# Kernel tuning notes

Measured on AMD Instinct MI355X. Metric: run time of the kernel, lower is better.

## Reference

```python
import jax, jax.numpy as jnp
import numpy as np

N, D = 4096, 512
TAU, ALPHA, EPS = 0.2, 0.5, 1e-15
L2_EPS = 1e-12  # F.normalize eps


def setup_inputs() -> dict:
    key = jax.random.key(0)
    ks = jax.random.split(key, 12)
    # xavier_normal_ with gain=1.414 for [D, D] linears
    std = 1.414 * (2.0 / (D + D)) ** 0.5
    xn = lambda k: jax.random.normal(k, (D, D), jnp.float32) * std
    return {
        "z1": jax.random.normal(ks[0], (N, D), jnp.float32),
        "z2": jax.random.normal(ks[1], (N, D), jnp.float32),
        # local projector: Linear -> PReLU -> Linear
        "lw1": xn(ks[2]), "lb1": jnp.zeros((D,), jnp.float32),
        "la": jnp.full((1,), 0.25, jnp.float32),  # PReLU weight (torch default 0.25)
        "lw2": xn(ks[3]), "lb2": jnp.zeros((D,), jnp.float32),
        # global projector
        "gw1": xn(ks[4]), "gb1": jnp.zeros((D,), jnp.float32),
        "ga": jnp.full((1,), 0.25, jnp.float32),
        "gw2": xn(ks[5]), "gb2": jnp.zeros((D,), jnp.float32),
        # discriminator bilinear weight
        "W": xn(ks[6]),
        # binary positive-pair mask [N, N]
        "mask": jax.random.randint(ks[7], (N, N), 0, 2, jnp.int32),
    }


def _prelu(x, a):
    return jnp.where(x >= 0, x, a * x)


def _proj(z, w1, b1, a, w2, b2):
    # nn.Sequential(Linear, PReLU, Linear); torch Linear: z @ W.T + b
    return _prelu(z @ w1.T + b1, a[0]) @ w2.T + b2


def _l2norm(z):
    n = jnp.linalg.norm(z, axis=-1, keepdims=True)
    return z / jnp.maximum(n, L2_EPS)


def _infonce(h1, h2, m, tau):
    a = _l2norm(h1)
    b = _l2norm(h2)
    sim_intra = jnp.exp(a @ a.T / tau)  # [N, N]
    sim_inter = jnp.exp(a @ b.T / tau)  # [N, N]
    num = (sim_inter * m).sum(1)
    den = sim_intra.sum(1) + sim_inter.sum(1) - (sim_intra * m).sum(1)
    return (-jnp.log(num / den)).mean()


def reference(z1, z2, lw1, lb1, la, lw2, lb2, gw1, gb1, ga, gw2, gb2, W, mask):
    m = mask.astype(jnp.float32)
    # local (node-level) InfoNCE through the local projector
    h1 = _proj(z1, lw1, lb1, la, lw2, lb2)
    h2 = _proj(z2, lw1, lb1, la, lw2, lb2)
    local = 0.5 * (_infonce(h1, h2, m, TAU) + _infonce(h2, h1, m.T, TAU))

    # global (DGI-style) loss
    def gloss(pos_z, neg_z):
        s = pos_z.mean(0)                               # readout [D]
        h = _proj(s, gw1, gb1, ga, gw2, gb2)            # global projector [D]
        summ = W @ h                                    # [D]
        d_pos = jax.nn.sigmoid(pos_z @ summ)            # [N]
        d_neg = jax.nn.sigmoid(neg_z @ summ)            # [N]
        pos_loss = -jnp.log(d_pos + EPS).mean()
        neg_loss = -jnp.log(1.0 - d_neg + EPS).mean()
        return 0.5 * (pos_loss + neg_loss)

    glob = 0.5 * (gloss(z1, z2) + gloss(z2, z1))
    return ALPHA * local + (1.0 - ALPHA) * glob
```

## Files before the change

### kernel.cpp

```cpp
#include <hip/hip_runtime.h>
#include <math.h>

#define NN 4096
#define DD 512
#define INV_TAU 5.0f
#define EPSV 1e-15f

typedef unsigned short u16;
typedef __attribute__((ext_vector_type(8))) short short8;
typedef __attribute__((ext_vector_type(4))) float f32x4;

__device__ __forceinline__ void gld16(const void* g, void* l) {
  __builtin_amdgcn_global_load_lds(
      (const __attribute__((address_space(1))) unsigned int*)g,
      (__attribute__((address_space(3))) unsigned int*)l, 16, 0, 0);
}

__device__ __forceinline__ float bf2f(u16 u) {
  return __uint_as_float(((unsigned)u) << 16);
}
__device__ __forceinline__ u16 f2bf(float x) {
  unsigned u = __float_as_uint(x);
  u += 0x7fff + ((u >> 16) & 1);
  return (u16)(u >> 16);
}

__device__ __forceinline__ float wave_sum(float v) {
#pragma unroll
  for (int o = 32; o > 0; o >>= 1) v += __shfl_down(v, o, 64);
  return v;
}

__global__ __launch_bounds__(256) void tobf16_2(const float* __restrict__ a,
                                                const float* __restrict__ b,
                                                u16* __restrict__ d,
                                                int n4each) {
  const int i = blockIdx.x * 256 + threadIdx.x;
  const float* s =
      (i < n4each) ? a + (size_t)i * 4 : b + (size_t)(i - n4each) * 4;
  float4 v = *(const float4*)s;
  unsigned long long pk = (unsigned long long)f2bf(v.x) |
                          ((unsigned long long)f2bf(v.y) << 16) |
                          ((unsigned long long)f2bf(v.z) << 32) |
                          ((unsigned long long)f2bf(v.w) << 48);
  *(unsigned long long*)&d[(size_t)i * 4] = pk;
}

template <int ACT>
__global__ __launch_bounds__(256) void gemm_mfma(
    const u16* __restrict__ A, const u16* __restrict__ Bw,
    const float* __restrict__ bias, const float* __restrict__ alpha_p,
    u16* __restrict__ out) {
  __shared__ __align__(16) u16 sA[2][128 * 32], sB[2][128 * 32];
  const int tid = threadIdx.x, w = tid >> 6, lane = tid & 63;
  const int rq = lane >> 2, cq = (lane & 3) * 8;
  const int quad = lane >> 4, m16 = lane & 15;
  const int wi = w >> 1, wj = w & 1;
  const int i0 = blockIdx.y * 128, j0 = blockIdx.x * 128;
  const u16* Ab = A + (size_t)blockIdx.z * ((size_t)NN * DD);
  u16* ob = out + (size_t)blockIdx.z * ((size_t)NN * DD);
  const int p = w >> 1, rh = (w & 1) * 64;
  const u16* gs = p ? Bw : Ab;
  const int grow0 = (p ? j0 : i0) + rh + rq;
  u16* lb0 = p ? &sB[0][rh * 32] : &sA[0][rh * 32];
  u16* lb1 = p ? &sB[1][rh * 32] : &sA[1][rh * 32];
#pragma unroll
  for (int rr = 0; rr < 64; rr += 16)
    gld16(&gs[(size_t)(grow0 + rr) * DD + cq], lb0 + rr * 32);
  f32x4 acc[4][4] = {};
  for (int kc = 0; kc < 16; ++kc) {
    __syncthreads();
    if (kc < 15) {
      const int kn = (kc + 1) * 32;
      u16* d = (kc & 1) ? lb0 : lb1;
#pragma unroll
      for (int rr = 0; rr < 64; rr += 16)
        gld16(&gs[(size_t)(grow0 + rr) * DD + kn + cq], d + rr * 32);
    }
    const u16* As = sA[kc & 1];
    const u16* Bs = sB[kc & 1];
    short8 ar[4], br[4];
#pragma unroll
    for (int s = 0; s < 4; ++s) {
      ar[s] = *(const short8*)&As[(wi * 64 + s * 16 + m16) * 32 + quad * 8];
      br[s] = *(const short8*)&Bs[(wj * 64 + s * 16 + m16) * 32 + quad * 8];
    }
#pragma unroll
    for (int si = 0; si < 4; ++si)
#pragma unroll
      for (int sj = 0; sj < 4; ++sj)
        acc[si][sj] = __builtin_amdgcn_mfma_f32_16x16x32_bf16(
            ar[si], br[sj], acc[si][sj], 0, 0, 0);
  }
  const float al = ACT ? alpha_p[0] : 0.f;
#pragma unroll
  for (int si = 0; si < 4; ++si)
#pragma unroll
    for (int sj = 0; sj < 4; ++sj) {
      const int col = j0 + wj * 64 + sj * 16 + m16;
      const float bv = bias[col];
#pragma unroll
      for (int r = 0; r < 4; ++r) {
        const int row = i0 + wi * 64 + si * 16 + quad * 4 + r;
        float x = acc[si][sj][r] + bv;
        if (ACT) x = (x >= 0.f) ? x : al * x;
        ob[(size_t)row * DD + col] = f2bf(x);
      }
    }
}

__global__ __launch_bounds__(256) void rownorm_bf16(const u16* __restrict__ h,
                                                    u16* __restrict__ o) {
  const int row = blockIdx.x;
  const int t = threadIdx.x;
  const size_t base = (size_t)row * DD;
  float v0 = bf2f(h[base + t]);
  float v1 = bf2f(h[base + 256 + t]);
  float s = v0 * v0 + v1 * v1;
  s = wave_sum(s);
  __shared__ float wsum[4];
  const int lane = t & 63, wid = t >> 6;
  if (lane == 0) wsum[wid] = s;
  __syncthreads();
  if (t == 0) {
    float tot = wsum[0] + wsum[1] + wsum[2] + wsum[3];
    wsum[0] = 1.f / fmaxf(sqrtf(tot), 1e-12f);
  }
  __syncthreads();
  const float inv = wsum[0];
  o[base + t] = f2bf(v0 * inv);
  o[base + 256 + t] = f2bf(v1 * inv);
}

__global__ __launch_bounds__(512) void sim_mfma(
    const u16* __restrict__ na, const u16* __restrict__ nb,
    const int* __restrict__ mask, float* __restrict__ zb) {
  __shared__ __align__(16) u16 sP[2][4][128 * 32];
  const int tid = threadIdx.x;
  const int w = tid >> 6, lane = tid & 63;
  const int rq = lane >> 2, cq = (lane & 3) * 8;
  const int quad = lane >> 4, m16 = lane & 15;
  const int ig = w & 3, jh = w >> 2;
  const int i0 = blockIdx.y * 128, j0 = blockIdx.x * 128;
  const int p = w >> 1, rh = (w & 1) * 64;
  const u16* gs = (p & 1) ? nb : na;
  const int grow0 = ((p < 2) ? i0 : j0) + rh + rq;
  u16* lb0 = &sP[0][p][rh * 32];
  u16* lb1 = &sP[1][p][rh * 32];
#pragma unroll
  for (int rr = 0; rr < 64; rr += 16)
    gld16(&gs[(size_t)(grow0 + rr) * DD + cq], lb0 + rr * 32);
  f32x4 a11[2][4] = {}, a12[2][4] = {}, a22[2][4] = {};
  for (int kc = 0; kc < 16; ++kc) {
    __syncthreads();
    if (kc < 15) {
      const int kn = (kc + 1) * 32;
      u16* d = (kc & 1) ? lb0 : lb1;
#pragma unroll
      for (int rr = 0; rr < 64; rr += 16)
        gld16(&gs[(size_t)(grow0 + rr) * DD + kn + cq], d + rr * 32);
    }
    const u16* Ai = sP[kc & 1][0];
    const u16* Bi = sP[kc & 1][1];
    const u16* Aj = sP[kc & 1][2];
    const u16* Bj = sP[kc & 1][3];
    short8 ai0 = *(const short8*)&Ai[(ig * 32 + m16) * 32 + quad * 8];
    short8 ai1 = *(const short8*)&Ai[(ig * 32 + 16 + m16) * 32 + quad * 8];
    short8 bi0 = *(const short8*)&Bi[(ig * 32 + m16) * 32 + quad * 8];
    short8 bi1 = *(const short8*)&Bi[(ig * 32 + 16 + m16) * 32 + quad * 8];
#pragma unroll
    for (int c = 0; c < 4; ++c) {
      short8 aj = *(const short8*)&Aj[(jh * 64 + c * 16 + m16) * 32 + quad * 8];
      short8 bj = *(const short8*)&Bj[(jh * 64 + c * 16 + m16) * 32 + quad * 8];
      a11[0][c] = __builtin_amdgcn_mfma_f32_16x16x32_bf16(ai0, aj, a11[0][c], 0, 0, 0);
      a11[1][c] = __builtin_amdgcn_mfma_f32_16x16x32_bf16(ai1, aj, a11[1][c], 0, 0, 0);
      a12[0][c] = __builtin_amdgcn_mfma_f32_16x16x32_bf16(ai0, bj, a12[0][c], 0, 0, 0);
      a12[1][c] = __builtin_amdgcn_mfma_f32_16x16x32_bf16(ai1, bj, a12[1][c], 0, 0, 0);
      a22[0][c] = __builtin_amdgcn_mfma_f32_16x16x32_bf16(bi0, bj, a22[0][c], 0, 0, 0);
      a22[1][c] = __builtin_amdgcn_mfma_f32_16x16x32_bf16(bi1, bj, a22[1][c], 0, 0, 0);
    }
  }
  float* rred = (float*)&sP[0][0][0];
  float* cred = rred + 512;
  rred[tid] = 0.f;
  rred[tid + 512] = 0.f;
  __syncthreads();
  float rs11[2][4] = {}, rm11[2][4] = {}, rs12[2][4] = {}, rm12[2][4] = {};
  float cs12[4] = {}, cm12[4] = {}, cs22[4] = {}, cm22[4] = {};
#pragma unroll
  for (int t = 0; t < 2; ++t)
#pragma unroll
    for (int c = 0; c < 4; ++c) {
      const int gj = j0 + jh * 64 + c * 16 + m16;
#pragma unroll
      for (int r = 0; r < 4; ++r) {
        const int gi = i0 + ig * 32 + t * 16 + quad * 4 + r;
        const float mv = (float)mask[(size_t)gi * NN + gj];
        const float e11 = __expf(a11[t][c][r] * INV_TAU);
        const float e12 = __expf(a12[t][c][r] * INV_TAU);
        const float e22 = __expf(a22[t][c][r] * INV_TAU);
        rs11[t][r] += e11;
        rm11[t][r] += e11 * mv;
        rs12[t][r] += e12;
        rm12[t][r] += e12 * mv;
        cs12[c] += e12;
        cm12[c] += e12 * mv;
        cs22[c] += e22;
        cm22[c] += e22 * mv;
      }
    }
#pragma unroll
  for (int t = 0; t < 2; ++t)
#pragma unroll
    for (int r = 0; r < 4; ++r) {
      float v0 = rs11[t][r], v1 = rm11[t][r], v2 = rs12[t][r], v3 = rm12[t][r];
#pragma unroll
      for (int o = 1; o < 16; o <<= 1) {
        v0 += __shfl_xor(v0, o, 64);
        v1 += __shfl_xor(v1, o, 64);
        v2 += __shfl_xor(v2, o, 64);
        v3 += __shfl_xor(v3, o, 64);
      }
      if (m16 == 0) {
        const int il = ig * 32 + t * 16 + quad * 4 + r;
        atomicAdd(&rred[0 * 128 + il], v0);
        atomicAdd(&rred[1 * 128 + il], v1);
        atomicAdd(&rred[2 * 128 + il], v2);
        atomicAdd(&rred[3 * 128 + il], v3);
      }
    }
#pragma unroll
  for (int c = 0; c < 4; ++c) {
    float v0 = cs12[c], v1 = cm12[c], v2 = cs22[c], v3 = cm22[c];
    v0 += __shfl_xor(v0, 16, 64); v0 += __shfl_xor(v0, 32, 64);
    v1 += __shfl_xor(v1, 16, 64); v1 += __shfl_xor(v1, 32, 64);
    v2 += __shfl_xor(v2, 16, 64); v2 += __shfl_xor(v2, 32, 64);
    v3 += __shfl_xor(v3, 16, 64); v3 += __shfl_xor(v3, 32, 64);
    if (lane < 16) {
      const int jl = jh * 64 + c * 16 + lane;
      atomicAdd(&cred[0 * 128 + jl], v0);
      atomicAdd(&cred[1 * 128 + jl], v1);
      atomicAdd(&cred[2 * 128 + jl], v2);
      atomicAdd(&cred[3 * 128 + jl], v3);
    }
  }
  __syncthreads();
  if (tid < 128) {
#pragma unroll
    for (int q = 0; q < 4; ++q)
      atomicAdd(&zb[q * NN + i0 + tid], rred[q * 128 + tid]);
  } else if (tid < 256) {
    const int jl = tid - 128;
#pragma unroll
    for (int q = 0; q < 4; ++q)
      atomicAdd(&zb[(4 + q) * NN + j0 + jl], cred[q * 128 + jl]);
  }
}

__global__ __launch_bounds__(256) void local_fin(const float* __restrict__ zb,
                                                 float* __restrict__ scal) {
  const int i = blockIdx.x * 256 + threadIdx.x;
  const float r11 = zb[i], r11m = zb[NN + i];
  const float r12 = zb[2 * NN + i], r12m = zb[3 * NN + i];
  const float c12 = zb[4 * NN + i], c12m = zb[5 * NN + i];
  const float c22 = zb[6 * NN + i], c22m = zb[7 * NN + i];
  float l1 = -logf(r12m / (r11 + r12 - r11m));
  float l2 = -logf(c12m / (c22 + c12 - c22m));
  l1 = wave_sum(l1);
  l2 = wave_sum(l2);
  __shared__ float b1[4], b2[4];
  const int lane = threadIdx.x & 63, wid = threadIdx.x >> 6;
  if (lane == 0) { b1[wid] = l1; b2[wid] = l2; }
  __syncthreads();
  if (threadIdx.x == 0) {
    atomicAdd(&scal[0], b1[0] + b1[1] + b1[2] + b1[3]);
    atomicAdd(&scal[1], b2[0] + b2[1] + b2[2] + b2[3]);
  }
}

__global__ __launch_bounds__(256) void colmean(const float* __restrict__ z1,
                                               const float* __restrict__ z2,
                                               float* __restrict__ s1,
                                               float* __restrict__ s2) {
  const int c = blockIdx.x * 256 + threadIdx.x;
  const int r0 = blockIdx.y * 64;
  float a = 0.f, b = 0.f;
  for (int r = r0; r < r0 + 64; ++r) {
    a += z1[(size_t)r * DD + c];
    b += z2[(size_t)r * DD + c];
  }
  atomicAdd(&s1[c], a * (1.f / NN));
  atomicAdd(&s2[c], b * (1.f / NN));
}

__global__ __launch_bounds__(256) void matvec2(
    const float* __restrict__ M, const float* __restrict__ x1,
    const float* __restrict__ x2, const float* __restrict__ bias,
    const float* __restrict__ alpha_p, int act, float* __restrict__ y1,
    float* __restrict__ y2) {
  const float* x = blockIdx.y ? x2 : x1;
  float* y = blockIdx.y ? y2 : y1;
  const int row = (blockIdx.x * 256 + threadIdx.x) >> 6;
  const int lane = threadIdx.x & 63;
  float acc = 0.f;
#pragma unroll
  for (int t = 0; t < 8; ++t)
    acc = fmaf(M[(size_t)row * DD + lane + 64 * t], x[lane + 64 * t], acc);
  acc = wave_sum(acc);
  if (lane == 0) {
    if (bias) acc += bias[row];
    if (act) { const float al = alpha_p[0]; acc = (acc >= 0.f) ? acc : al * acc; }
    y[row] = acc;
  }
}

__global__ __launch_bounds__(256) void logsig2(
    const float* __restrict__ z1, const float* __restrict__ z2,
    const float* __restrict__ sm1, const float* __restrict__ sm2,
    float* __restrict__ scal) {
  const int ch = blockIdx.y;
  const float* z = ch ? z2 : z1;
  const float* sp = ch ? sm2 : sm1;
  const float* sn = ch ? sm1 : sm2;
  float* accP = ch ? &scal[4] : &scal[2];
  float* accN = ch ? &scal[3] : &scal[5];
  const int lane = threadIdx.x & 63;
  const int wid = threadIdx.x >> 6;
  const int row = blockIdx.x * 4 + wid;
  float dp = 0.f, dn = 0.f;
#pragma unroll
  for (int t = 0; t < 8; ++t) {
    const float zv = z[(size_t)row * DD + lane + 64 * t];
    dp = fmaf(zv, sp[lane + 64 * t], dp);
    dn = fmaf(zv, sn[lane + 64 * t], dn);
  }
  dp = wave_sum(dp);
  dn = wave_sum(dn);
  __shared__ float bp[4], bn[4];
  if (lane == 0) {
    const float sg = 1.f / (1.f + __expf(-dp));
    bp[wid] = -logf(sg + EPSV);
    const float sg2 = 1.f / (1.f + __expf(-dn));
    bn[wid] = -logf(1.f - sg2 + EPSV);
  }
  __syncthreads();
  if (threadIdx.x == 0) {
    atomicAdd(accP, bp[0] + bp[1] + bp[2] + bp[3]);
    atomicAdd(accN, bn[0] + bn[1] + bn[2] + bn[3]);
  }
}

__global__ void combine(const float* __restrict__ scal, float* __restrict__ out) {
  const float local = 0.5f * (scal[0] + scal[1]) * (1.f / NN);
  const float glob = 0.25f * (scal[2] + scal[3] + scal[4] + scal[5]) * (1.f / NN);
  out[0] = 0.5f * local + 0.5f * glob;
}

extern "C" void kernel_launch(void* const* d_in, const int* in_sizes, int n_in,
                              void* d_out, int out_size, void* d_ws,
                              size_t ws_size, hipStream_t stream) {
  const float* z1 = (const float*)d_in[0];
  const float* z2 = (const float*)d_in[1];
  const float* lw1 = (const float*)d_in[2];
  const float* lb1 = (const float*)d_in[3];
  const float* la = (const float*)d_in[4];
  const float* lw2 = (const float*)d_in[5];
  const float* lb2 = (const float*)d_in[6];
  const float* gw1 = (const float*)d_in[7];
  const float* gb1 = (const float*)d_in[8];
  const float* ga = (const float*)d_in[9];
  const float* gw2 = (const float*)d_in[10];
  const float* gb2 = (const float*)d_in[11];
  const float* W = (const float*)d_in[12];
  const int* mask = (const int*)d_in[13];
  float* out = (float*)d_out;

  const size_t ND = (size_t)NN * DD;
  u16* W1b = (u16*)d_ws;
  u16* W2b = W1b + 512 * 512;
  u16* Ab = W1b + 2 * 512 * 512;
  u16* Bb = Ab + 2 * ND;
  float* zbf = (float*)(Bb + 2 * ND);
  float* s1 = zbf + 8 * NN;
  float* s2 = s1 + DD;
  float* scal = s2 + DD;
  float* t1 = scal + 16;
  float* hg1 = t1 + DD;
  float* summ1 = hg1 + DD;
  float* t2 = summ1 + DD;
  float* hg2 = t2 + DD;
  float* summ2 = hg2 + DD;

  hipMemsetAsync(zbf, 0, (8 * NN + 2 * DD + 16) * sizeof(float), stream);

  dim3 blk(256);
  tobf16_2<<<512, blk, 0, stream>>>(lw1, lw2, W1b, 512 * 512 / 4);
  tobf16_2<<<4096, blk, 0, stream>>>(z1, z2, Ab, (int)(ND / 4));

  dim3 gg(4, 32, 2);
  gemm_mfma<1><<<gg, blk, 0, stream>>>(Ab, W1b, lb1, la, Bb);
  gemm_mfma<0><<<gg, blk, 0, stream>>>(Bb, W2b, lb2, la, Ab);
  rownorm_bf16<<<2 * NN, blk, 0, stream>>>(Ab, Bb);

  sim_mfma<<<dim3(NN / 128, NN / 128), dim3(512), 0, stream>>>(Bb, Bb + ND,
                                                               mask, zbf);
  local_fin<<<NN / 256, blk, 0, stream>>>(zbf, scal);

  colmean<<<dim3(DD / 256, 64), blk, 0, stream>>>(z1, z2, s1, s2);
  matvec2<<<dim3(DD / 4, 2), blk, 0, stream>>>(gw1, s1, s2, gb1, ga, 1, t1, t2);
  matvec2<<<dim3(DD / 4, 2), blk, 0, stream>>>(gw2, t1, t2, gb2, nullptr, 0, hg1, hg2);
  matvec2<<<dim3(DD / 4, 2), blk, 0, stream>>>(W, hg1, hg2, nullptr, nullptr, 0, summ1, summ2);
  logsig2<<<dim3(NN / 4, 2), blk, 0, stream>>>(z1, z2, summ1, summ2, scal);

  combine<<<1, 1, 0, stream>>>(scal, out);
}
```

Measured before the change: 309.1 us.

## Fuse prep and global chain, fold row norms into sim epilogue, retile GEMMs

Merges the bf16 conversions and column-mean into one prep kernel, and collapses the three matvec launches into a single two-block globchain kernel. The normalized-embedding pass is replaced by a per-row inverse-norm vector that the similarity epilogue applies inside the exponent. sim_mfma moves from 512 to 256 threads, each wave computing a larger 64x64 tile. The projector GEMM uses 128x64 tiles. logsig2 reads the bf16 copy of z instead of fp32. This cuts launches and memory passes, but lowers precision in the global dot products, raises register pressure in the similarity kernel, and runs globchain serially on only two blocks.

```diff
diff --git a/kernel.cpp b/kernel.cpp
--- a/kernel.cpp
+++ b/kernel.cpp
@@ -31,19 +31,50 @@
   return v;
 }
 
-__global__ __launch_bounds__(256) void tobf16_2(const float* __restrict__ a,
-                                                const float* __restrict__ b,
-                                                u16* __restrict__ d,
-                                                int n4each) {
-  const int i = blockIdx.x * 256 + threadIdx.x;
-  const float* s =
-      (i < n4each) ? a + (size_t)i * 4 : b + (size_t)(i - n4each) * 4;
-  float4 v = *(const float4*)s;
-  unsigned long long pk = (unsigned long long)f2bf(v.x) |
-                          ((unsigned long long)f2bf(v.y) << 16) |
-                          ((unsigned long long)f2bf(v.z) << 32) |
-                          ((unsigned long long)f2bf(v.w) << 48);
-  *(unsigned long long*)&d[(size_t)i * 4] = pk;
+__global__ __launch_bounds__(256) void prep(
+    const float* __restrict__ z1, const float* __restrict__ z2,
+    const float* __restrict__ lw1, const float* __restrict__ lw2,
+    u16* __restrict__ Ab, u16* __restrict__ Wb, float* __restrict__ s1,
+    float* __restrict__ s2) {
+  const int tid = threadIdx.x;
+  if (blockIdx.y == 2) {
+#pragma unroll
+    for (int k = 0; k < 8; ++k) {
+      const int idx = blockIdx.x * 256 + tid + k * 16384;
+      const float* s = (idx < 65536) ? &lw1[(size_t)idx * 4]
+                                     : &lw2[(size_t)(idx - 65536) * 4];
+      float4 v = *(const float4*)s;
+      unsigned long long pk = (unsigned long long)f2bf(v.x) |
+                              ((unsigned long long)f2bf(v.y) << 16) |
+                              ((unsigned long long)f2bf(v.z) << 32) |
+                              ((unsigned long long)f2bf(v.w) << 48);
+      *(unsigned long long*)&Wb[(size_t)idx * 4] = pk;
+    }
+    return;
+  }
+  const float* z = blockIdx.y ? z2 : z1;
+  u16* dst = Ab + (size_t)blockIdx.y * ((size_t)NN * DD);
+  float* sdst = blockIdx.y ? s2 : s1;
+  const int col4 = tid & 127;
+  const int rg = tid >> 7;
+  const int r0 = blockIdx.x * 64;
+  float4 acc = make_float4(0.f, 0.f, 0.f, 0.f);
+#pragma unroll 4
+  for (int k = 0; k < 32; ++k) {
+    const int r = r0 + rg + k * 2;
+    float4 v = *(const float4*)&z[(size_t)r * DD + col4 * 4];
+    acc.x += v.x; acc.y += v.y; acc.z += v.z; acc.w += v.w;
+    unsigned long long pk = (unsigned long long)f2bf(v.x) |
+                            ((unsigned long long)f2bf(v.y) << 16) |
+                            ((unsigned long long)f2bf(v.z) << 32) |
+                            ((unsigned long long)f2bf(v.w) << 48);
+    *(unsigned long long*)&dst[(size_t)r * DD + col4 * 4] = pk;
+  }
+  const float inv = 1.f / NN;
+  atomicAdd(&sdst[col4 * 4 + 0], acc.x * inv);
+  atomicAdd(&sdst[col4 * 4 + 1], acc.y * inv);
+  atomicAdd(&sdst[col4 * 4 + 2], acc.z * inv);
+  atomicAdd(&sdst[col4 * 4 + 3], acc.w * inv);
 }
 
 template <int ACT>
@@ -51,53 +82,55 @@
     const u16* __restrict__ A, const u16* __restrict__ Bw,
     const float* __restrict__ bias, const float* __restrict__ alpha_p,
     u16* __restrict__ out) {
-  __shared__ __align__(16) u16 sA[2][128 * 32], sB[2][128 * 32];
+  __shared__ __align__(16) u16 sA[2][128 * 32], sB[2][64 * 32];
   const int tid = threadIdx.x, w = tid >> 6, lane = tid & 63;
   const int rq = lane >> 2, cq = (lane & 3) * 8;
   const int quad = lane >> 4, m16 = lane & 15;
   const int wi = w >> 1, wj = w & 1;
-  const int i0 = blockIdx.y * 128, j0 = blockIdx.x * 128;
-  const u16* Ab = A + (size_t)blockIdx.z * ((size_t)NN * DD);
+  const int i0 = blockIdx.y * 128, j0 = blockIdx.x * 64;
+  const u16* Apan = A + (size_t)blockIdx.z * ((size_t)NN * DD);
   u16* ob = out + (size_t)blockIdx.z * ((size_t)NN * DD);
-  const int p = w >> 1, rh = (w & 1) * 64;
-  const u16* gs = p ? Bw : Ab;
-  const int grow0 = (p ? j0 : i0) + rh + rq;
-  u16* lb0 = p ? &sB[0][rh * 32] : &sA[0][rh * 32];
-  u16* lb1 = p ? &sB[1][rh * 32] : &sA[1][rh * 32];
-#pragma unroll
-  for (int rr = 0; rr < 64; rr += 16)
-    gld16(&gs[(size_t)(grow0 + rr) * DD + cq], lb0 + rr * 32);
-  f32x4 acc[4][4] = {};
+  const bool st = (w < 3);
+  const u16* gs = (w == 2) ? Bw : Apan;
+  const int gr0 = (w == 2) ? (j0 + rq) : (i0 + (w == 1 ? 64 : 0) + rq);
+  u16* lb0 = (w == 2) ? sB[0] : &sA[0][(w == 1 ? 64 : 0) * 32];
+  u16* lb1 = (w == 2) ? sB[1] : &sA[1][(w == 1 ? 64 : 0) * 32];
+  if (st) {
+#pragma unroll
+    for (int rr = 0; rr < 64; rr += 16)
+      gld16(&gs[(size_t)(gr0 + rr) * DD + cq], lb0 + rr * 32);
+  }
+  f32x4 acc[4][2] = {};
   for (int kc = 0; kc < 16; ++kc) {
     __syncthreads();
-    if (kc < 15) {
+    if (kc < 15 && st) {
       const int kn = (kc + 1) * 32;
       u16* d = (kc & 1) ? lb0 : lb1;
 #pragma unroll
       for (int rr = 0; rr < 64; rr += 16)
-        gld16(&gs[(size_t)(grow0 + rr) * DD + kn + cq], d + rr * 32);
+        gld16(&gs[(size_t)(gr0 + rr) * DD + kn + cq], d + rr * 32);
     }
     const u16* As = sA[kc & 1];
     const u16* Bs = sB[kc & 1];
-    short8 ar[4], br[4];
-#pragma unroll
-    for (int s = 0; s < 4; ++s) {
-      ar[s] = *(const short8*)&As[(wi * 64 + s * 16 + m16) * 32 + quad * 8];
-      br[s] = *(const short8*)&Bs[(wj * 64 + s * 16 + m16) * 32 + quad * 8];
-    }
-#pragma unroll
-    for (int si = 0; si < 4; ++si)
-#pragma unroll
-      for (int sj = 0; sj < 4; ++sj)
+    short8 bj[2];
+#pragma unroll
+    for (int sj = 0; sj < 2; ++sj)
+      bj[sj] = *(const short8*)&Bs[(wj * 32 + sj * 16 + m16) * 32 + quad * 8];
+#pragma unroll
+    for (int si = 0; si < 4; ++si) {
+      short8 ai = *(const short8*)&As[(wi * 64 + si * 16 + m16) * 32 + quad * 8];
+#pragma unroll
+      for (int sj = 0; sj < 2; ++sj)
         acc[si][sj] = __builtin_amdgcn_mfma_f32_16x16x32_bf16(
-            ar[si], br[sj], acc[si][sj], 0, 0, 0);
+            ai, bj[sj], acc[si][sj], 0, 0, 0);
+    }
   }
   const float al = ACT ? alpha_p[0] : 0.f;
 #pragma unroll
   for (int si = 0; si < 4; ++si)
 #pragma unroll
-    for (int sj = 0; sj < 4; ++sj) {
-      const int col = j0 + wj * 64 + sj * 16 + m16;
+    for (int sj = 0; sj < 2; ++sj) {
+      const int col = j0 + wj * 32 + sj * 16 + m16;
       const float bv = bias[col];
 #pragma unroll
       for (int r = 0; r < 4; ++r) {
@@ -109,111 +142,110 @@
     }
 }
 
-__global__ __launch_bounds__(256) void rownorm_bf16(const u16* __restrict__ h,
-                                                    u16* __restrict__ o) {
-  const int row = blockIdx.x;
-  const int t = threadIdx.x;
-  const size_t base = (size_t)row * DD;
-  float v0 = bf2f(h[base + t]);
-  float v1 = bf2f(h[base + 256 + t]);
-  float s = v0 * v0 + v1 * v1;
+__global__ __launch_bounds__(256) void rowinvnorm(const u16* __restrict__ h,
+                                                  float* __restrict__ invn) {
+  const int row = blockIdx.x * 4 + (threadIdx.x >> 6);
+  const int lane = threadIdx.x & 63;
+  short8 v = *(const short8*)&h[(size_t)row * DD + lane * 8];
+  float s = 0.f;
+#pragma unroll
+  for (int k = 0; k < 8; ++k) {
+    const float f = bf2f(((const u16*)&v)[k]);
+    s += f * f;
+  }
   s = wave_sum(s);
-  __shared__ float wsum[4];
-  const int lane = t & 63, wid = t >> 6;
-  if (lane == 0) wsum[wid] = s;
-  __syncthreads();
-  if (t == 0) {
-    float tot = wsum[0] + wsum[1] + wsum[2] + wsum[3];
-    wsum[0] = 1.f / fmaxf(sqrtf(tot), 1e-12f);
-  }
-  __syncthreads();
-  const float inv = wsum[0];
-  o[base + t] = f2bf(v0 * inv);
-  o[base + 256 + t] = f2bf(v1 * inv);
-}
-
-__global__ __launch_bounds__(512) void sim_mfma(
+  if (lane == 0) invn[row] = 1.f / fmaxf(sqrtf(s), 1e-12f);
+}
+
+__global__ __launch_bounds__(256, 2) void sim_mfma(
     const u16* __restrict__ na, const u16* __restrict__ nb,
+    const float* __restrict__ invA, const float* __restrict__ invB,
     const int* __restrict__ mask, float* __restrict__ zb) {
   __shared__ __align__(16) u16 sP[2][4][128 * 32];
-  const int tid = threadIdx.x;
-  const int w = tid >> 6, lane = tid & 63;
+  const int tid = threadIdx.x, w = tid >> 6, lane = tid & 63;
   const int rq = lane >> 2, cq = (lane & 3) * 8;
   const int quad = lane >> 4, m16 = lane & 15;
-  const int ig = w & 3, jh = w >> 2;
+  const int wi = w >> 1, wj = w & 1;
   const int i0 = blockIdx.y * 128, j0 = blockIdx.x * 128;
-  const int p = w >> 1, rh = (w & 1) * 64;
-  const u16* gs = (p & 1) ? nb : na;
-  const int grow0 = ((p < 2) ? i0 : j0) + rh + rq;
-  u16* lb0 = &sP[0][p][rh * 32];
-  u16* lb1 = &sP[1][p][rh * 32];
-#pragma unroll
-  for (int rr = 0; rr < 64; rr += 16)
-    gld16(&gs[(size_t)(grow0 + rr) * DD + cq], lb0 + rr * 32);
-  f32x4 a11[2][4] = {}, a12[2][4] = {}, a22[2][4] = {};
+  const u16* gs = (w & 1) ? nb : na;
+  const int gr0 = ((w < 2) ? i0 : j0) + rq;
+  u16* lb0 = &sP[0][w][0];
+  u16* lb1 = &sP[1][w][0];
+#pragma unroll
+  for (int rr = 0; rr < 128; rr += 16)
+    gld16(&gs[(size_t)(gr0 + rr) * DD + cq], lb0 + rr * 32);
+  f32x4 a11[4][4] = {}, a12[4][4] = {}, a22[4][4] = {};
   for (int kc = 0; kc < 16; ++kc) {
     __syncthreads();
     if (kc < 15) {
       const int kn = (kc + 1) * 32;
       u16* d = (kc & 1) ? lb0 : lb1;
 #pragma unroll
-      for (int rr = 0; rr < 64; rr += 16)
-        gld16(&gs[(size_t)(grow0 + rr) * DD + kn + cq], d + rr * 32);
+      for (int rr = 0; rr < 128; rr += 16)
+        gld16(&gs[(size_t)(gr0 + rr) * DD + kn + cq], d + rr * 32);
     }
     const u16* Ai = sP[kc & 1][0];
     const u16* Bi = sP[kc & 1][1];
     const u16* Aj = sP[kc & 1][2];
     const u16* Bj = sP[kc & 1][3];
-    short8 ai0 = *(const short8*)&Ai[(ig * 32 + m16) * 32 + quad * 8];
-    short8 ai1 = *(const short8*)&Ai[(ig * 32 + 16 + m16) * 32 + quad * 8];
-    short8 bi0 = *(const short8*)&Bi[(ig * 32 + m16) * 32 + quad * 8];
-    short8 bi1 = *(const short8*)&Bi[(ig * 32 + 16 + m16) * 32 + quad * 8];
-#pragma unroll
-    for (int c = 0; c < 4; ++c) {
-      short8 aj = *(const short8*)&Aj[(jh * 64 + c * 16 + m16) * 32 + quad * 8];
-      short8 bj = *(const short8*)&Bj[(jh * 64 + c * 16 + m16) * 32 + quad * 8];
-      a11[0][c] = __builtin_amdgcn_mfma_f32_16x16x32_bf16(ai0, aj, a11[0][c], 0, 0, 0);
-      a11[1][c] = __builtin_amdgcn_mfma_f32_16x16x32_bf16(ai1, aj, a11[1][c], 0, 0, 0);
-      a12[0][c] = __builtin_amdgcn_mfma_f32_16x16x32_bf16(ai0, bj, a12[0][c], 0, 0, 0);
-      a12[1][c] = __builtin_amdgcn_mfma_f32_16x16x32_bf16(ai1, bj, a12[1][c], 0, 0, 0);
-      a22[0][c] = __builtin_amdgcn_mfma_f32_16x16x32_bf16(bi0, bj, a22[0][c], 0, 0, 0);
-      a22[1][c] = __builtin_amdgcn_mfma_f32_16x16x32_bf16(bi1, bj, a22[1][c], 0, 0, 0);
-    }
-  }
+    short8 aj[4], bj[4];
+#pragma unroll
+    for (int sj = 0; sj < 4; ++sj) {
+      aj[sj] = *(const short8*)&Aj[(wj * 64 + sj * 16 + m16) * 32 + quad * 8];
+      bj[sj] = *(const short8*)&Bj[(wj * 64 + sj * 16 + m16) * 32 + quad * 8];
+    }
+#pragma unroll
+    for (int si = 0; si < 4; ++si) {
+      short8 ai = *(const short8*)&Ai[(wi * 64 + si * 16 + m16) * 32 + quad * 8];
+      short8 bi = *(const short8*)&Bi[(wi * 64 + si * 16 + m16) * 32 + quad * 8];
+#pragma unroll
+      for (int sj = 0; sj < 4; ++sj) {
+        a11[si][sj] = __builtin_amdgcn_mfma_f32_16x16x32_bf16(ai, aj[sj], a11[si][sj], 0, 0, 0);
+        a12[si][sj] = __builtin_amdgcn_mfma_f32_16x16x32_bf16(ai, bj[sj], a12[si][sj], 0, 0, 0);
+        a22[si][sj] = __builtin_amdgcn_mfma_f32_16x16x32_bf16(bi, bj[sj], a22[si][sj], 0, 0, 0);
+      }
+    }
+  }
+  __syncthreads();
   float* rred = (float*)&sP[0][0][0];
   float* cred = rred + 512;
-  rred[tid] = 0.f;
-  rred[tid + 512] = 0.f;
-  __syncthreads();
-  float rs11[2][4] = {}, rm11[2][4] = {}, rs12[2][4] = {}, rm12[2][4] = {};
+  rred[tid] = 0.f; rred[tid + 256] = 0.f;
+  rred[tid + 512] = 0.f; rred[tid + 768] = 0.f;
+  __syncthreads();
+  float4 iAr[4], iBr[4];
+  float iAc[4], iBc[4];
+#pragma unroll
+  for (int s = 0; s < 4; ++s) {
+    iAr[s] = *(const float4*)&invA[i0 + wi * 64 + s * 16 + quad * 4];
+    iBr[s] = *(const float4*)&invB[i0 + wi * 64 + s * 16 + quad * 4];
+    iAc[s] = invA[j0 + wj * 64 + s * 16 + m16];
+    iBc[s] = invB[j0 + wj * 64 + s * 16 + m16];
+  }
   float cs12[4] = {}, cm12[4] = {}, cs22[4] = {}, cm22[4] = {};
 #pragma unroll
-  for (int t = 0; t < 2; ++t)
-#pragma unroll
-    for (int c = 0; c < 4; ++c) {
-      const int gj = j0 + jh * 64 + c * 16 + m16;
+  for (int si = 0; si < 4; ++si) {
+    float rs11[4] = {}, rm11[4] = {}, rs12[4] = {}, rm12[4] = {};
+    const float ia4[4] = {iAr[si].x, iAr[si].y, iAr[si].z, iAr[si].w};
+    const float ib4[4] = {iBr[si].x, iBr[si].y, iBr[si].z, iBr[si].w};
+#pragma unroll
+    for (int sj = 0; sj < 4; ++sj) {
+      const int gj = j0 + wj * 64 + sj * 16 + m16;
 #pragma unroll
       for (int r = 0; r < 4; ++r) {
-        const int gi = i0 + ig * 32 + t * 16 + quad * 4 + r;
+        const int gi = i0 + wi * 64 + si * 16 + quad * 4 + r;
         const float mv = (float)mask[(size_t)gi * NN + gj];
-        const float e11 = __expf(a11[t][c][r] * INV_TAU);
-        const float e12 = __expf(a12[t][c][r] * INV_TAU);
-        const float e22 = __expf(a22[t][c][r] * INV_TAU);
-        rs11[t][r] += e11;
-        rm11[t][r] += e11 * mv;
-        rs12[t][r] += e12;
-        rm12[t][r] += e12 * mv;
-        cs12[c] += e12;
-        cm12[c] += e12 * mv;
-        cs22[c] += e22;
-        cm22[c] += e22 * mv;
+        const float e11 = __expf(a11[si][sj][r] * ia4[r] * iAc[sj] * INV_TAU);
+        const float e12 = __expf(a12[si][sj][r] * ia4[r] * iBc[sj] * INV_TAU);
+        const float e22 = __expf(a22[si][sj][r] * ib4[r] * iBc[sj] * INV_TAU);
+        rs11[r] += e11; rm11[r] += e11 * mv;
+        rs12[r] += e12; rm12[r] += e12 * mv;
+        cs12[sj] += e12; cm12[sj] += e12 * mv;
+        cs22[sj] += e22; cm22[sj] += e22 * mv;
       }
     }
 #pragma unroll
-  for (int t = 0; t < 2; ++t)
-#pragma unroll
     for (int r = 0; r < 4; ++r) {
-      float v0 = rs11[t][r], v1 = rm11[t][r], v2 = rs12[t][r], v3 = rm12[t][r];
+      float v0 = rs11[r], v1 = rm11[r], v2 = rs12[r], v3 = rm12[r];
 #pragma unroll
       for (int o = 1; o < 16; o <<= 1) {
         v0 += __shfl_xor(v0, o, 64);
@@ -222,22 +254,23 @@
         v3 += __shfl_xor(v3, o, 64);
       }
       if (m16 == 0) {
-        const int il = ig * 32 + t * 16 + quad * 4 + r;
+        const int il = wi * 64 + si * 16 + quad * 4 + r;
         atomicAdd(&rred[0 * 128 + il], v0);
         atomicAdd(&rred[1 * 128 + il], v1);
         atomicAdd(&rred[2 * 128 + il], v2);
         atomicAdd(&rred[3 * 128 + il], v3);
       }
     }
-#pragma unroll
-  for (int c = 0; c < 4; ++c) {
-    float v0 = cs12[c], v1 = cm12[c], v2 = cs22[c], v3 = cm22[c];
+  }
+#pragma unroll
+  for (int sj = 0; sj < 4; ++sj) {
+    float v0 = cs12[sj], v1 = cm12[sj], v2 = cs22[sj], v3 = cm22[sj];
     v0 += __shfl_xor(v0, 16, 64); v0 += __shfl_xor(v0, 32, 64);
     v1 += __shfl_xor(v1, 16, 64); v1 += __shfl_xor(v1, 32, 64);
     v2 += __shfl_xor(v2, 16, 64); v2 += __shfl_xor(v2, 32, 64);
     v3 += __shfl_xor(v3, 16, 64); v3 += __shfl_xor(v3, 32, 64);
     if (lane < 16) {
-      const int jl = jh * 64 + c * 16 + lane;
+      const int jl = wj * 64 + sj * 16 + lane;
       atomicAdd(&cred[0 * 128 + jl], v0);
       atomicAdd(&cred[1 * 128 + jl], v1);
       atomicAdd(&cred[2 * 128 + jl], v2);
@@ -249,7 +282,7 @@
 #pragma unroll
     for (int q = 0; q < 4; ++q)
       atomicAdd(&zb[q * NN + i0 + tid], rred[q * 128 + tid]);
-  } else if (tid < 256) {
+  } else {
     const int jl = tid - 128;
 #pragma unroll
     for (int q = 0; q < 4; ++q)
@@ -278,75 +311,91 @@
   }
 }
 
-__global__ __launch_bounds__(256) void colmean(const float* __restrict__ z1,
-                                               const float* __restrict__ z2,
-                                               float* __restrict__ s1,
-                                               float* __restrict__ s2) {
-  const int c = blockIdx.x * 256 + threadIdx.x;
-  const int r0 = blockIdx.y * 64;
-  float a = 0.f, b = 0.f;
-  for (int r = r0; r < r0 + 64; ++r) {
-    a += z1[(size_t)r * DD + c];
-    b += z2[(size_t)r * DD + c];
-  }
-  atomicAdd(&s1[c], a * (1.f / NN));
-  atomicAdd(&s2[c], b * (1.f / NN));
-}
-
-__global__ __launch_bounds__(256) void matvec2(
-    const float* __restrict__ M, const float* __restrict__ x1,
-    const float* __restrict__ x2, const float* __restrict__ bias,
-    const float* __restrict__ alpha_p, int act, float* __restrict__ y1,
-    float* __restrict__ y2) {
-  const float* x = blockIdx.y ? x2 : x1;
-  float* y = blockIdx.y ? y2 : y1;
-  const int row = (blockIdx.x * 256 + threadIdx.x) >> 6;
-  const int lane = threadIdx.x & 63;
-  float acc = 0.f;
-#pragma unroll
-  for (int t = 0; t < 8; ++t)
-    acc = fmaf(M[(size_t)row * DD + lane + 64 * t], x[lane + 64 * t], acc);
-  acc = wave_sum(acc);
-  if (lane == 0) {
-    if (bias) acc += bias[row];
-    if (act) { const float al = alpha_p[0]; acc = (acc >= 0.f) ? acc : al * acc; }
-    y[row] = acc;
-  }
+__global__ __launch_bounds__(256) void globchain(
+    const float* __restrict__ gw1, const float* __restrict__ gb1,
+    const float* __restrict__ ga, const float* __restrict__ gw2,
+    const float* __restrict__ gb2, const float* __restrict__ Wd,
+    const float* __restrict__ s1, const float* __restrict__ s2,
+    float* __restrict__ summ1, float* __restrict__ summ2) {
+  __shared__ float xv[512], tv[512];
+  const int ch = blockIdx.x;
+  const float* s = ch ? s2 : s1;
+  float* outp = ch ? summ2 : summ1;
+  const int tid = threadIdx.x;
+  const int r1 = tid, r2 = tid + 256;
+  xv[r1] = s[r1];
+  xv[r2] = s[r2];
+  __syncthreads();
+  const float al = ga[0];
+  float d0 = 0.f, d1 = 0.f;
+  for (int k = 0; k < 512; k += 4) {
+    float4 a = *(const float4*)&gw1[(size_t)r1 * 512 + k];
+    float4 b = *(const float4*)&gw1[(size_t)r2 * 512 + k];
+    d0 += a.x * xv[k] + a.y * xv[k + 1] + a.z * xv[k + 2] + a.w * xv[k + 3];
+    d1 += b.x * xv[k] + b.y * xv[k + 1] + b.z * xv[k + 2] + b.w * xv[k + 3];
+  }
+  d0 += gb1[r1]; d1 += gb1[r2];
+  tv[r1] = (d0 >= 0.f) ? d0 : al * d0;
+  tv[r2] = (d1 >= 0.f) ? d1 : al * d1;
+  __syncthreads();
+  d0 = 0.f; d1 = 0.f;
+  for (int k = 0; k < 512; k += 4) {
+    float4 a = *(const float4*)&gw2[(size_t)r1 * 512 + k];
+    float4 b = *(const float4*)&gw2[(size_t)r2 * 512 + k];
+    d0 += a.x * tv[k] + a.y * tv[k + 1] + a.z * tv[k + 2] + a.w * tv[k + 3];
+    d1 += b.x * tv[k] + b.y * tv[k + 1] + b.z * tv[k + 2] + b.w * tv[k + 3];
+  }
+  __syncthreads();
+  xv[r1] = d0 + gb2[r1];
+  xv[r2] = d1 + gb2[r2];
+  __syncthreads();
+  d0 = 0.f; d1 = 0.f;
+  for (int k = 0; k < 512; k += 4) {
+    float4 a = *(const float4*)&Wd[(size_t)r1 * 512 + k];
+    float4 b = *(const float4*)&Wd[(size_t)r2 * 512 + k];
+    d0 += a.x * xv[k] + a.y * xv[k + 1] + a.z * xv[k + 2] + a.w * xv[k + 3];
+    d1 += b.x * xv[k] + b.y * xv[k + 1] + b.z * xv[k + 2] + b.w * xv[k + 3];
+  }
+  outp[r1] = d0;
+  outp[r2] = d1;
 }
 
 __global__ __launch_bounds__(256) void logsig2(
-    const float* __restrict__ z1, const float* __restrict__ z2,
-    const float* __restrict__ sm1, const float* __restrict__ sm2,
-    float* __restrict__ scal) {
+    const u16* __restrict__ zb16, const float* __restrict__ sm1,
+    const float* __restrict__ sm2, float* __restrict__ scal) {
   const int ch = blockIdx.y;
-  const float* z = ch ? z2 : z1;
+  const u16* z = zb16 + (size_t)ch * ((size_t)NN * DD);
   const float* sp = ch ? sm2 : sm1;
   const float* sn = ch ? sm1 : sm2;
-  float* accP = ch ? &scal[4] : &scal[2];
-  float* accN = ch ? &scal[3] : &scal[5];
-  const int lane = threadIdx.x & 63;
-  const int wid = threadIdx.x >> 6;
-  const int row = blockIdx.x * 4 + wid;
-  float dp = 0.f, dn = 0.f;
-#pragma unroll
-  for (int t = 0; t < 8; ++t) {
-    const float zv = z[(size_t)row * DD + lane + 64 * t];
-    dp = fmaf(zv, sp[lane + 64 * t], dp);
-    dn = fmaf(zv, sn[lane + 64 * t], dn);
-  }
-  dp = wave_sum(dp);
-  dn = wave_sum(dn);
-  __shared__ float bp[4], bn[4];
+  const int lane = threadIdx.x & 63, wv = threadIdx.x >> 6;
+  float sp8[8], sn8[8];
+#pragma unroll
+  for (int k = 0; k < 8; ++k) {
+    sp8[k] = sp[lane * 8 + k];
+    sn8[k] = sn[lane * 8 + k];
+  }
+  float accP = 0.f, accN = 0.f;
+#pragma unroll
+  for (int rr = 0; rr < 4; ++rr) {
+    const int row = blockIdx.x * 16 + wv * 4 + rr;
+    short8 v = *(const short8*)&z[(size_t)row * DD + lane * 8];
+    float dp = 0.f, dn = 0.f;
+#pragma unroll
+    for (int k = 0; k < 8; ++k) {
+      const float f = bf2f(((const u16*)&v)[k]);
+      dp = fmaf(f, sp8[k], dp);
+      dn = fmaf(f, sn8[k], dn);
+    }
+    dp = wave_sum(dp);
+    dn = wave_sum(dn);
+    if (lane == 0) {
+      accP += -logf(1.f / (1.f + __expf(-dp)) + EPSV);
+      accN += -logf(1.f - 1.f / (1.f + __expf(-dn)) + EPSV);
+    }
+  }
   if (lane == 0) {
-    const float sg = 1.f / (1.f + __expf(-dp));
-    bp[wid] = -logf(sg + EPSV);
-    const float sg2 = 1.f / (1.f + __expf(-dn));
-    bn[wid] = -logf(1.f - sg2 + EPSV);
-  }
-  __syncthreads();
-  if (threadIdx.x == 0) {
-    atomicAdd(accP, bp[0] + bp[1] + bp[2] + bp[3]);
-    atomicAdd(accN, bn[0] + bn[1] + bn[2] + bn[3]);
+    atomicAdd(&scal[ch ? 4 : 2], accP);
+    atomicAdd(&scal[ch ? 3 : 5], accN);
   }
 }
 
@@ -379,38 +428,33 @@
   u16* W1b = (u16*)d_ws;
   u16* W2b = W1b + 512 * 512;
   u16* Ab = W1b + 2 * 512 * 512;
-  u16* Bb = Ab + 2 * ND;
-  float* zbf = (float*)(Bb + 2 * ND);
+  u16* Pb = Ab + 2 * ND;
+  u16* Hb = Pb + 2 * ND;
+  float* invn = (float*)(Hb + 2 * ND);
+  float* zbf = invn + 2 * NN;
   float* s1 = zbf + 8 * NN;
   float* s2 = s1 + DD;
   float* scal = s2 + DD;
-  float* t1 = scal + 16;
-  float* hg1 = t1 + DD;
-  float* summ1 = hg1 + DD;
-  float* t2 = summ1 + DD;
-  float* hg2 = t2 + DD;
-  float* summ2 = hg2 + DD;
+  float* summ1 = scal + 16;
+  float* summ2 = summ1 + DD;
 
   hipMemsetAsync(zbf, 0, (8 * NN + 2 * DD + 16) * sizeof(float), stream);
 
   dim3 blk(256);
-  tobf16_2<<<512, blk, 0, stream>>>(lw1, lw2, W1b, 512 * 512 / 4);
-  tobf16_2<<<4096, blk, 0, stream>>>(z1, z2, Ab, (int)(ND / 4));
-
-  dim3 gg(4, 32, 2);
-  gemm_mfma<1><<<gg, blk, 0, stream>>>(Ab, W1b, lb1, la, Bb);
-  gemm_mfma<0><<<gg, blk, 0, stream>>>(Bb, W2b, lb2, la, Ab);
-  rownorm_bf16<<<2 * NN, blk, 0, stream>>>(Ab, Bb);
-
-  sim_mfma<<<dim3(NN / 128, NN / 128), dim3(512), 0, stream>>>(Bb, Bb + ND,
-                                                               mask, zbf);
+  prep<<<dim3(64, 3), blk, 0, stream>>>(z1, z2, lw1, lw2, Ab, W1b, s1, s2);
+
+  dim3 gg(8, 32, 2);
+  gemm_mfma<1><<<gg, blk, 0, stream>>>(Ab, W1b, lb1, la, Pb);
+  gemm_mfma<0><<<gg, blk, 0, stream>>>(Pb, W2b, lb2, la, Hb);
+  rowinvnorm<<<2 * NN / 4, blk, 0, stream>>>(Hb, invn);
+
+  sim_mfma<<<dim3(NN / 128, NN / 128), blk, 0, stream>>>(
+      Hb, Hb + ND, invn, invn + NN, mask, zbf);
   local_fin<<<NN / 256, blk, 0, stream>>>(zbf, scal);
 
-  colmean<<<dim3(DD / 256, 64), blk, 0, stream>>>(z1, z2, s1, s2);
-  matvec2<<<dim3(DD / 4, 2), blk, 0, stream>>>(gw1, s1, s2, gb1, ga, 1, t1, t2);
-  matvec2<<<dim3(DD / 4, 2), blk, 0, stream>>>(gw2, t1, t2, gb2, nullptr, 0, hg1, hg2);
-  matvec2<<<dim3(DD / 4, 2), blk, 0, stream>>>(W, hg1, hg2, nullptr, nullptr, 0, summ1, summ2);
-  logsig2<<<dim3(NN / 4, 2), blk, 0, stream>>>(z1, z2, summ1, summ2, scal);
+  globchain<<<2, blk, 0, stream>>>(gw1, gb1, ga, gw2, gb2, W, s1, s2, summ1,
+                                   summ2);
+  logsig2<<<dim3(NN / 16, 2), blk, 0, stream>>>(Ab, summ1, summ2, scal);
 
   combine<<<1, 1, 0, stream>>>(scal, out);
 }
```

New measurement: 445.0 us. 44.0% more time.
